# Kernel optimization log

Hardware: AMD Instinct MI355X
Metric: run time of the kernel (lower is better)

The kernel has to match this reference:

```python
import jax, jax.numpy as jnp
import numpy as np

N_EXPERT_CAPACITY = 2  # init kwarg; k = S * capacity // E


def setup_inputs() -> dict:
    key = jax.random.key(0)
    k1, k2, k3, k4 = jax.random.split(key, 4)
    B, S, D, E, F = 8, 1024, 1024, 8, 2048
    # kaiming-uniform-ish scales
    x = jax.random.normal(k1, (B, S, D), dtype=jnp.float32)
    choice_w = jax.random.uniform(k2, (E, D), dtype=jnp.float32, minval=-1.0, maxval=1.0) * (1.0 / np.sqrt(D))
    w1 = jax.random.uniform(k3, (E, D, F), dtype=jnp.float32, minval=-1.0, maxval=1.0) * (1.0 / np.sqrt(D))
    w2 = jax.random.uniform(k4, (E, F, D), dtype=jnp.float32, minval=-1.0, maxval=1.0) * (1.0 / np.sqrt(F))
    return {"x": x, "choice_w": choice_w, "w1": w1, "w2": w2}


def reference(x, choice_w, w1, w2):
    B, S, D = x.shape
    E = choice_w.shape[0]
    k = S * N_EXPERT_CAPACITY // E  # tokens per expert (expert-choice)
    # router softmax over experts: [B, S, E]
    probs = jax.nn.softmax(jnp.einsum('bsd,ed->bse', x, choice_w), axis=-1)
    # each expert picks its top-k tokens: G, I are [B, E, k]
    G, I = jax.lax.top_k(jnp.swapaxes(probs, -1, -2), k)
    # dispatch: gather tokens instead of one-hot matmul (same math)
    x_in = jnp.take_along_axis(x[:, None, :, :], I[..., None], axis=2)  # [B, E, k, D]
    # per-expert MLP with SiLU
    h = jax.nn.silu(jnp.einsum('bekd,edf->bekf', x_in, w1))  # [B, E, k, F]
    x_mlp = jnp.einsum('bekf,efd->bekd', h, w2)              # [B, E, k, D]
    # combine: weighted scatter-add back to token positions (equals P,G,x_mlp einsum)
    b_idx = jnp.arange(B)[:, None, None]  # [B,1,1] broadcasts with I [B,E,k]
    out = jnp.zeros_like(x).at[b_idx, I].add(G[..., None] * x_mlp)
    return out
```

## Files before the change

### kernel.cpp

```cpp
#include <hip/hip_runtime.h>
#include <hip/hip_bf16.h>
#include <math.h>

#define B_   8
#define S_   1024
#define D_   1024
#define E_   8
#define F_   2048
#define KCAP 256

typedef __bf16 bf16x8 __attribute__((ext_vector_type(8)));
typedef float  floatx4 __attribute__((ext_vector_type(4)));
typedef unsigned short ushortx8 __attribute__((ext_vector_type(8)));

__device__ __forceinline__ unsigned short f2b(float f) {
    union { float f; unsigned int u; } v; v.f = f;
    unsigned int u = v.u;
    u += 0x7fffu + ((u >> 16) & 1u);
    return (unsigned short)(u >> 16);
}
__device__ __forceinline__ float b2f(unsigned short u) {
    union { unsigned int u; float f; } v; v.u = ((unsigned)u) << 16; return v.f;
}

__device__ __forceinline__ void gl_lds16(const void* g, void* l) {
    __builtin_amdgcn_global_load_lds(
        (const __attribute__((address_space(1))) void*)g,
        (__attribute__((address_space(3))) void*)l, 16, 0, 0);
}

__device__ __forceinline__ unsigned long long topk_key(float p, int s) {
    return (((unsigned long long)__float_as_uint(p)) << 10) | (unsigned)(S_ - 1 - s);
}

__global__ void router_kernel(const float* __restrict__ x, const float* __restrict__ cw,
                              float* __restrict__ probs, unsigned short* __restrict__ xb) {
    int gid  = blockIdx.x * 256 + threadIdx.x;
    int wave = gid >> 6;
    int lane = gid & 63;
    int b = wave >> 10;
    int s = wave & (S_ - 1);
    const float* xrow = x + ((size_t)b * S_ + s) * D_;
    unsigned short* xbrow = xb + ((size_t)b * S_ + s) * D_;
    float acc[E_];
#pragma unroll
    for (int e = 0; e < E_; e++) acc[e] = 0.f;
#pragma unroll
    for (int it = 0; it < D_ / 256; it++) {
        int i = it * 256 + lane * 4;
        float4 xv = *(const float4*)(xrow + i);
        ushort4 o;
        o.x = f2b(xv.x); o.y = f2b(xv.y); o.z = f2b(xv.z); o.w = f2b(xv.w);
        *(ushort4*)(xbrow + i) = o;
#pragma unroll
        for (int e = 0; e < E_; e++) {
            float4 wv = *(const float4*)(cw + e * D_ + i);
            acc[e] = fmaf(xv.x, wv.x, fmaf(xv.y, wv.y, fmaf(xv.z, wv.z, fmaf(xv.w, wv.w, acc[e]))));
        }
    }
#pragma unroll
    for (int e = 0; e < E_; e++) {
        float v = acc[e];
#pragma unroll
        for (int off = 32; off >= 1; off >>= 1) v += __shfl_down(v, off, 64);
        acc[e] = v;
    }
    if (lane == 0) {
        float m = acc[0];
#pragma unroll
        for (int e = 1; e < E_; e++) m = fmaxf(m, acc[e]);
        float sum = 0.f;
#pragma unroll
        for (int e = 0; e < E_; e++) { acc[e] = __expf(acc[e] - m); sum += acc[e]; }
        float inv = 1.f / sum;
#pragma unroll
        for (int e = 0; e < E_; e++) probs[((size_t)b * E_ + e) * S_ + s] = acc[e] * inv;
    }
}

union PrepSm {
    float tile[2][128][33];
    unsigned long long keys[S_];
};

#define PREP_DECODE(T, INP, OUTP, RV, CV, C0, R0) do { \
    int t_ = (T); \
    if (t_ < 4096) { \
        int e_ = t_ >> 9, tt_ = t_ & 511; \
        INP = w1 + (size_t)e_ * D_ * F_;  OUTP = w1t + (size_t)e_ * D_ * F_; \
        RV = D_; CV = F_; C0 = (tt_ & 63) * 32; R0 = (tt_ >> 6) * 128; \
    } else { \
        int t2_ = t_ - 4096; \
        int e_ = t2_ >> 9, tt_ = t2_ & 511; \
        INP = w2 + (size_t)e_ * D_ * F_;  OUTP = w2t + (size_t)e_ * D_ * F_; \
        RV = F_; CV = D_; C0 = (tt_ & 31) * 32; R0 = (tt_ >> 5) * 128; \
    } \
} while (0)

__global__ void prep_kernel(const float* __restrict__ w1, const float* __restrict__ w2,
                            unsigned short* __restrict__ w1t, unsigned short* __restrict__ w2t,
                            const float* __restrict__ probs, int* __restrict__ I,
                            float* __restrict__ G, unsigned short* __restrict__ Pmap) {
    const int bid = blockIdx.x;
    const int tid = threadIdx.x;
    __shared__ PrepSm sm;

    if (bid < B_ * E_) {
        const int be = bid;
        const int b = be >> 3, e = be & 7;
        const float* rowp = probs + (size_t)be * S_;
#pragma unroll
        for (int q = 0; q < 4; q++) {
            const int s = q * 256 + tid;
            sm.keys[s] = topk_key(rowp[s], s);
            Pmap[((size_t)(b * S_ + s)) * E_ + e] = 0;
        }
        __syncthreads();
        unsigned long long my[4];
        int r[4] = {0, 0, 0, 0};
#pragma unroll
        for (int q = 0; q < 4; q++) my[q] = sm.keys[q * 256 + tid];
#pragma unroll 8
        for (int t = 0; t < S_; t++) {
            const unsigned long long kt = sm.keys[t];
#pragma unroll
            for (int q = 0; q < 4; q++) r[q] += (kt > my[q]);
        }
#pragma unroll
        for (int q = 0; q < 4; q++) {
            if (r[q] < KCAP) {
                const int s = q * 256 + tid;
                I[be * KCAP + r[q]] = s;
                G[be * KCAP + r[q]] = rowp[s];
                Pmap[((size_t)(b * S_ + s)) * E_ + e] = (unsigned short)(r[q] + 1);
            }
        }
        return;
    }

    const int tb   = bid - B_ * E_;
    const int lrow = tid >> 3;
    const int seg  = tid & 7;
    const int c    = tid >> 3;
    const int k    = tid & 7;

    const float* inp; unsigned short* outp; int R, C, c0, r0;
    PREP_DECODE(tb, inp, outp, R, C, c0, r0);
    float4 v[4];
#pragma unroll
    for (int i = 0; i < 4; i++)
        v[i] = *(const float4*)(inp + (size_t)(r0 + lrow + i * 32) * C + c0 + seg * 4);

    int buf = 0;
    for (int T = tb; T < 8192; T += 768) {
        unsigned short* oute = outp;
        const int Rr = R, cc0 = c0, rr0 = r0;

#pragma unroll
        for (int i = 0; i < 4; i++) {
            const int rr = lrow + i * 32;
            sm.tile[buf][rr][seg * 4 + 0] = v[i].x;
            sm.tile[buf][rr][seg * 4 + 1] = v[i].y;
            sm.tile[buf][rr][seg * 4 + 2] = v[i].z;
            sm.tile[buf][rr][seg * 4 + 3] = v[i].w;
        }
        if (T + 768 < 8192) {
            PREP_DECODE(T + 768, inp, outp, R, C, c0, r0);
#pragma unroll
            for (int i = 0; i < 4; i++)
                v[i] = *(const float4*)(inp + (size_t)(r0 + lrow + i * 32) * C + c0 + seg * 4);
        }
        __builtin_amdgcn_sched_barrier(0);
        asm volatile("s_waitcnt lgkmcnt(0)" ::: "memory");
        __builtin_amdgcn_s_barrier();
        __builtin_amdgcn_sched_barrier(0);
#pragma unroll
        for (int srep = 0; srep < 2; srep++) {
            const int s8 = k + srep * 8;
            ushortx8 o;
#pragma unroll
            for (int j = 0; j < 8; j++) o[j] = f2b(sm.tile[buf][s8 * 8 + j][c]);
            *(ushortx8*)(oute + (size_t)(cc0 + c) * Rr + rr0 + s8 * 8) = o;
        }
        buf ^= 1;
    }
}


__global__ __launch_bounds__(256, 4) void gemm1_kernel(
    const unsigned short* __restrict__ xb,
    const unsigned short* __restrict__ w1t,
    const int* __restrict__ I,
    unsigned short* __restrict__ H)
{
    const int g  = blockIdx.x;
    const int e  = g & 7;
    const int rr = g >> 3;
    const int b  = rr >> 5;
    const int t5 = rr & 31;
    const int be = b * 8 + e;
    const int mt = t5 & 1;
    const int nt = t5 >> 1;
    const int tid = threadIdx.x;

    __shared__ __align__(16) unsigned short Asm[128 * 64];
    __shared__ __align__(16) unsigned short Bsm[128 * 64];
    __shared__ unsigned int ArowS[128];

    if (tid < 128) {
        int tok = I[(size_t)be * KCAP + mt * 128 + tid];
        ArowS[tid] = (unsigned)((b * S_ + tok) * D_);
    }
    __syncthreads();

    const int r8   = tid >> 3;
    const int kseg = (tid & 7) ^ (r8 & 7);
    unsigned aoffW[4];
#pragma unroll
    for (int w = 0; w < 4; w++) aoffW[w] = ArowS[w * 32 + r8] + kseg * 8;
    const size_t boff0 = ((size_t)e * F_ + nt * 128 + r8) * D_ + kseg * 8;

    const int lane = tid & 63;
    const int wv   = tid >> 6;
    const int wm   = (wv & 1) * 64;
    const int wn   = (wv >> 1) * 64;
    const int l15  = lane & 15;
    const int quad = lane >> 4;
    const int x0   = (quad ^ (l15 & 7)) * 8;

    int aoffs[4], boffs[4];
#pragma unroll
    for (int i = 0; i < 4; i++) {
        aoffs[i] = (wm + i * 16 + l15) * 64 + x0;
        boffs[i] = (wn + i * 16 + l15) * 64 + x0;
    }

    floatx4 acc[4][4];
#pragma unroll
    for (int i = 0; i < 4; i++)
#pragma unroll
        for (int j = 0; j < 4; j++) acc[i][j] = (floatx4){0.f, 0.f, 0.f, 0.f};

    for (int k0 = 0; k0 < D_; k0 += 64) {
#pragma unroll
        for (int w = 0; w < 4; w++) {
            gl_lds16(xb  + aoffW[w] + k0,                    &Asm[(w * 256 + tid) * 8]);
            gl_lds16(w1t + boff0 + (size_t)w * 32 * D_ + k0, &Bsm[(w * 256 + tid) * 8]);
        }
        __syncthreads();
        bf16x8 af[4], bfr[4];
#pragma unroll
        for (int i = 0; i < 4; i++) {
            af[i]  = *(const bf16x8*)&Asm[aoffs[i]];
            bfr[i] = *(const bf16x8*)&Bsm[boffs[i]];
        }
#pragma unroll
        for (int i = 0; i < 4; i++)
#pragma unroll
            for (int j = 0; j < 4; j++)
                acc[i][j] = __builtin_amdgcn_mfma_f32_16x16x32_bf16(af[i], bfr[j], acc[i][j], 0, 0, 0);
#pragma unroll
        for (int i = 0; i < 4; i++) {
            af[i]  = *(const bf16x8*)&Asm[aoffs[i] ^ 32];
            bfr[i] = *(const bf16x8*)&Bsm[boffs[i] ^ 32];
        }
#pragma unroll
        for (int i = 0; i < 4; i++)
#pragma unroll
            for (int j = 0; j < 4; j++)
                acc[i][j] = __builtin_amdgcn_mfma_f32_16x16x32_bf16(af[i], bfr[j], acc[i][j], 0, 0, 0);
        __syncthreads();
    }

    unsigned short* Hbe = H + (size_t)be * KCAP * F_;
#pragma unroll
    for (int i = 0; i < 4; i++) {
#pragma unroll
        for (int r = 0; r < 4; r++) {
            int m = mt * 128 + wm + i * 16 + quad * 4 + r;
            unsigned short* hrow = Hbe + (size_t)m * F_ + nt * 128;
#pragma unroll
            for (int j = 0; j < 4; j++) {
                float v = acc[i][j][r];
                float sv = v / (1.f + __expf(-v));
                hrow[wn + j * 16 + l15] = f2b(sv);
            }
        }
    }
}

__global__ __launch_bounds__(256, 4) void gemm2_kernel(
    const unsigned short* __restrict__ H,
    const unsigned short* __restrict__ w2t,
    unsigned short* __restrict__ xmlp)
{
    const int g  = blockIdx.x;
    const int e  = g & 7;
    const int rr = g >> 3;
    const int b  = rr >> 4;
    const int t4 = rr & 15;
    const int be = b * 8 + e;
    const int mt = t4 & 1;
    const int nt = t4 >> 1;
    const int tid = threadIdx.x;

    __shared__ __align__(16) unsigned short Asm2[128 * 64];
    __shared__ __align__(16) unsigned short Bsm2[128 * 64];

    const int r8   = tid >> 3;
    const int kseg = (tid & 7) ^ (r8 & 7);
    const size_t aoff0 = ((size_t)be * KCAP + mt * 128 + r8) * F_ + kseg * 8;
    const size_t boff0 = ((size_t)e * D_ + nt * 128 + r8) * F_ + kseg * 8;

    const int lane = tid & 63;
    const int wv   = tid >> 6;
    const int wm   = (wv & 1) * 64;
    const int wn   = (wv >> 1) * 64;
    const int l15  = lane & 15;
    const int quad = lane >> 4;
    const int x0   = (quad ^ (l15 & 7)) * 8;

    int aoffs[4], boffs[4];
#pragma unroll
    for (int i = 0; i < 4; i++) {
        aoffs[i] = (wm + i * 16 + l15) * 64 + x0;
        boffs[i] = (wn + i * 16 + l15) * 64 + x0;
    }

    floatx4 acc[4][4];
#pragma unroll
    for (int i = 0; i < 4; i++)
#pragma unroll
        for (int j = 0; j < 4; j++) acc[i][j] = (floatx4){0.f, 0.f, 0.f, 0.f};

    for (int k0 = 0; k0 < F_; k0 += 64) {
#pragma unroll
        for (int w = 0; w < 4; w++) {
            gl_lds16(H   + aoff0 + (size_t)w * 32 * F_ + k0, &Asm2[(w * 256 + tid) * 8]);
            gl_lds16(w2t + boff0 + (size_t)w * 32 * F_ + k0, &Bsm2[(w * 256 + tid) * 8]);
        }
        __syncthreads();
        bf16x8 af[4], bfr[4];
#pragma unroll
        for (int i = 0; i < 4; i++) {
            af[i]  = *(const bf16x8*)&Asm2[aoffs[i]];
            bfr[i] = *(const bf16x8*)&Bsm2[boffs[i]];
        }
#pragma unroll
        for (int i = 0; i < 4; i++)
#pragma unroll
            for (int j = 0; j < 4; j++)
                acc[i][j] = __builtin_amdgcn_mfma_f32_16x16x32_bf16(af[i], bfr[j], acc[i][j], 0, 0, 0);
#pragma unroll
        for (int i = 0; i < 4; i++) {
            af[i]  = *(const bf16x8*)&Asm2[aoffs[i] ^ 32];
            bfr[i] = *(const bf16x8*)&Bsm2[boffs[i] ^ 32];
        }
#pragma unroll
        for (int i = 0; i < 4; i++)
#pragma unroll
            for (int j = 0; j < 4; j++)
                acc[i][j] = __builtin_amdgcn_mfma_f32_16x16x32_bf16(af[i], bfr[j], acc[i][j], 0, 0, 0);
        __syncthreads();
    }

    unsigned short* Xbe = xmlp + (size_t)be * KCAP * D_;
#pragma unroll
    for (int i = 0; i < 4; i++) {
#pragma unroll
        for (int r = 0; r < 4; r++) {
            int m = mt * 128 + wm + i * 16 + quad * 4 + r;
            unsigned short* orow = Xbe + (size_t)m * D_ + nt * 128;
#pragma unroll
            for (int j = 0; j < 4; j++)
                orow[wn + j * 16 + l15] = f2b(acc[i][j][r]);
        }
    }
}

__global__ void combine_kernel(const unsigned short* __restrict__ xmlp,
                               const unsigned short* __restrict__ Pmap,
                               const float* __restrict__ G,
                               float* __restrict__ out) {
    int gid  = blockIdx.x * 256 + threadIdx.x;
    int wave = gid >> 6;
    int lane = gid & 63;
    int b = wave >> 10;
    float acc[16];
#pragma unroll
    for (int i = 0; i < 16; i++) acc[i] = 0.f;
    const unsigned short* pm = Pmap + (size_t)wave * E_;
#pragma unroll
    for (int e = 0; e < E_; e++) {
        int pe = pm[e];
        if (pe) {
            int beslot = (b * E_ + e) * KCAP + (pe - 1);
            float g = G[beslot];
            const unsigned short* rw = xmlp + (size_t)beslot * D_ + lane * 16;
            ushortx8 r0 = *(const ushortx8*)(rw);
            ushortx8 r1 = *(const ushortx8*)(rw + 8);
#pragma unroll
            for (int i = 0; i < 8; i++) {
                acc[i]     = fmaf(g, b2f(r0[i]), acc[i]);
                acc[8 + i] = fmaf(g, b2f(r1[i]), acc[8 + i]);
            }
        }
    }
    float* orow = out + (size_t)wave * D_ + lane * 16;
    ((float4*)orow)[0] = make_float4(acc[0],  acc[1],  acc[2],  acc[3]);
    ((float4*)orow)[1] = make_float4(acc[4],  acc[5],  acc[6],  acc[7]);
    ((float4*)orow)[2] = make_float4(acc[8],  acc[9],  acc[10], acc[11]);
    ((float4*)orow)[3] = make_float4(acc[12], acc[13], acc[14], acc[15]);
}

extern "C" void kernel_launch(void* const* d_in, const int* in_sizes, int n_in,
                              void* d_out, int out_size, void* d_ws, size_t ws_size,
                              hipStream_t stream) {
    const float* x  = (const float*)d_in[0];
    const float* cw = (const float*)d_in[1];
    const float* w1 = (const float*)d_in[2];
    const float* w2 = (const float*)d_in[3];
    float* out = (float*)d_out;

    char* ws = (char*)d_ws;
    float*          probs = (float*)(ws);
    int*            Ibuf  = (int*)(ws + 262144);
    float*          Gbuf  = (float*)(ws + 327680);
    unsigned short* Pmap  = (unsigned short*)(ws + 393216);
    unsigned short* xb    = (unsigned short*)(ws + 524288);
    unsigned short* w1t   = (unsigned short*)(ws + 17301504);
    unsigned short* xmlp  = w1t;
    unsigned short* w2t   = (unsigned short*)(ws + 50855936);
    unsigned short* Hbuf  = (unsigned short*)(ws + 84410368);

    router_kernel<<<(B_ * S_ * 64) / 256, 256, 0, stream>>>(x, cw, probs, xb);
    prep_kernel<<<B_ * E_ + 768, 256, 0, stream>>>(w1, w2, w1t, w2t, probs, Ibuf, Gbuf, Pmap);
    gemm1_kernel<<<B_ * E_ * 2 * (F_ / 128), 256, 0, stream>>>(xb, w1t, Ibuf, Hbuf);
    gemm2_kernel<<<B_ * E_ * 2 * (D_ / 128), 256, 0, stream>>>(Hbuf, w2t, xmlp);
    combine_kernel<<<(B_ * S_ * 64) / 256, 256, 0, stream>>>(xmlp, Pmap, Gbuf, out);
}
```

Baseline: 355.4 us.

## Overlap weight transposes with router and gemm1 by splitting prep work across kernels

The w1 transpose now runs inside the router kernel as extra persistent blocks, and the w2 transpose runs inside the gemm1 kernel as extra blocks. Top-k selection moves into its own small kernel. The goal is to hide the weight conversion and transpose traffic behind the router and gemm1 work instead of running it as a serial prep stage. In exchange, the transpose blocks compete with gemm1 for CUs and bandwidth, gemm1 now uses a larger shared-memory union, and there is one extra kernel launch.

```diff
diff --git a/kernel.cpp b/kernel.cpp
--- a/kernel.cpp
+++ b/kernel.cpp
@@ -32,56 +32,6 @@
 __device__ __forceinline__ unsigned long long topk_key(float p, int s) {
     return (((unsigned long long)__float_as_uint(p)) << 10) | (unsigned)(S_ - 1 - s);
 }
-
-__global__ void router_kernel(const float* __restrict__ x, const float* __restrict__ cw,
-                              float* __restrict__ probs, unsigned short* __restrict__ xb) {
-    int gid  = blockIdx.x * 256 + threadIdx.x;
-    int wave = gid >> 6;
-    int lane = gid & 63;
-    int b = wave >> 10;
-    int s = wave & (S_ - 1);
-    const float* xrow = x + ((size_t)b * S_ + s) * D_;
-    unsigned short* xbrow = xb + ((size_t)b * S_ + s) * D_;
-    float acc[E_];
-#pragma unroll
-    for (int e = 0; e < E_; e++) acc[e] = 0.f;
-#pragma unroll
-    for (int it = 0; it < D_ / 256; it++) {
-        int i = it * 256 + lane * 4;
-        float4 xv = *(const float4*)(xrow + i);
-        ushort4 o;
-        o.x = f2b(xv.x); o.y = f2b(xv.y); o.z = f2b(xv.z); o.w = f2b(xv.w);
-        *(ushort4*)(xbrow + i) = o;
-#pragma unroll
-        for (int e = 0; e < E_; e++) {
-            float4 wv = *(const float4*)(cw + e * D_ + i);
-            acc[e] = fmaf(xv.x, wv.x, fmaf(xv.y, wv.y, fmaf(xv.z, wv.z, fmaf(xv.w, wv.w, acc[e]))));
-        }
-    }
-#pragma unroll
-    for (int e = 0; e < E_; e++) {
-        float v = acc[e];
-#pragma unroll
-        for (int off = 32; off >= 1; off >>= 1) v += __shfl_down(v, off, 64);
-        acc[e] = v;
-    }
-    if (lane == 0) {
-        float m = acc[0];
-#pragma unroll
-        for (int e = 1; e < E_; e++) m = fmaxf(m, acc[e]);
-        float sum = 0.f;
-#pragma unroll
-        for (int e = 0; e < E_; e++) { acc[e] = __expf(acc[e] - m); sum += acc[e]; }
-        float inv = 1.f / sum;
-#pragma unroll
-        for (int e = 0; e < E_; e++) probs[((size_t)b * E_ + e) * S_ + s] = acc[e] * inv;
-    }
-}
-
-union PrepSm {
-    float tile[2][128][33];
-    unsigned long long keys[S_];
-};
 
 #define PREP_DECODE(T, INP, OUTP, RV, CV, C0, R0) do { \
     int t_ = (T); \
@@ -97,75 +47,37 @@
     } \
 } while (0)
 
-__global__ void prep_kernel(const float* __restrict__ w1, const float* __restrict__ w2,
-                            unsigned short* __restrict__ w1t, unsigned short* __restrict__ w2t,
-                            const float* __restrict__ probs, int* __restrict__ I,
-                            float* __restrict__ G, unsigned short* __restrict__ Pmap) {
-    const int bid = blockIdx.x;
-    const int tid = threadIdx.x;
-    __shared__ PrepSm sm;
-
-    if (bid < B_ * E_) {
-        const int be = bid;
-        const int b = be >> 3, e = be & 7;
-        const float* rowp = probs + (size_t)be * S_;
-#pragma unroll
-        for (int q = 0; q < 4; q++) {
-            const int s = q * 256 + tid;
-            sm.keys[s] = topk_key(rowp[s], s);
-            Pmap[((size_t)(b * S_ + s)) * E_ + e] = 0;
-        }
-        __syncthreads();
-        unsigned long long my[4];
-        int r[4] = {0, 0, 0, 0};
-#pragma unroll
-        for (int q = 0; q < 4; q++) my[q] = sm.keys[q * 256 + tid];
-#pragma unroll 8
-        for (int t = 0; t < S_; t++) {
-            const unsigned long long kt = sm.keys[t];
-#pragma unroll
-            for (int q = 0; q < 4; q++) r[q] += (kt > my[q]);
-        }
-#pragma unroll
-        for (int q = 0; q < 4; q++) {
-            if (r[q] < KCAP) {
-                const int s = q * 256 + tid;
-                I[be * KCAP + r[q]] = s;
-                G[be * KCAP + r[q]] = rowp[s];
-                Pmap[((size_t)(b * S_ + s)) * E_ + e] = (unsigned short)(r[q] + 1);
-            }
-        }
-        return;
-    }
-
-    const int tb   = bid - B_ * E_;
+__device__ __forceinline__ void transpose_persist(
+    const float* __restrict__ w1, const float* __restrict__ w2,
+    unsigned short* __restrict__ w1t, unsigned short* __restrict__ w2t,
+    float (*tile)[128][33], int T0, int Tend, int stride, int tid)
+{
     const int lrow = tid >> 3;
     const int seg  = tid & 7;
     const int c    = tid >> 3;
     const int k    = tid & 7;
 
     const float* inp; unsigned short* outp; int R, C, c0, r0;
-    PREP_DECODE(tb, inp, outp, R, C, c0, r0);
+    PREP_DECODE(T0, inp, outp, R, C, c0, r0);
     float4 v[4];
 #pragma unroll
     for (int i = 0; i < 4; i++)
         v[i] = *(const float4*)(inp + (size_t)(r0 + lrow + i * 32) * C + c0 + seg * 4);
 
     int buf = 0;
-    for (int T = tb; T < 8192; T += 768) {
+    for (int T = T0; T < Tend; T += stride) {
         unsigned short* oute = outp;
         const int Rr = R, cc0 = c0, rr0 = r0;
-
 #pragma unroll
         for (int i = 0; i < 4; i++) {
             const int rr = lrow + i * 32;
-            sm.tile[buf][rr][seg * 4 + 0] = v[i].x;
-            sm.tile[buf][rr][seg * 4 + 1] = v[i].y;
-            sm.tile[buf][rr][seg * 4 + 2] = v[i].z;
-            sm.tile[buf][rr][seg * 4 + 3] = v[i].w;
-        }
-        if (T + 768 < 8192) {
-            PREP_DECODE(T + 768, inp, outp, R, C, c0, r0);
+            tile[buf][rr][seg * 4 + 0] = v[i].x;
+            tile[buf][rr][seg * 4 + 1] = v[i].y;
+            tile[buf][rr][seg * 4 + 2] = v[i].z;
+            tile[buf][rr][seg * 4 + 3] = v[i].w;
+        }
+        if (T + stride < Tend) {
+            PREP_DECODE(T + stride, inp, outp, R, C, c0, r0);
 #pragma unroll
             for (int i = 0; i < 4; i++)
                 v[i] = *(const float4*)(inp + (size_t)(r0 + lrow + i * 32) * C + c0 + seg * 4);
@@ -179,21 +91,131 @@
             const int s8 = k + srep * 8;
             ushortx8 o;
 #pragma unroll
-            for (int j = 0; j < 8; j++) o[j] = f2b(sm.tile[buf][s8 * 8 + j][c]);
+            for (int j = 0; j < 8; j++) o[j] = f2b(tile[buf][s8 * 8 + j][c]);
             *(ushortx8*)(oute + (size_t)(cc0 + c) * Rr + rr0 + s8 * 8) = o;
         }
         buf ^= 1;
     }
 }
 
-
-__global__ __launch_bounds__(256, 4) void gemm1_kernel(
+__global__ void router_w1t_kernel(const float* __restrict__ x, const float* __restrict__ cw,
+                                  float* __restrict__ probs, unsigned short* __restrict__ xb,
+                                  const float* __restrict__ w1, const float* __restrict__ w2,
+                                  unsigned short* __restrict__ w1t, unsigned short* __restrict__ w2t) {
+    const int bid = blockIdx.x;
+    const int tid = threadIdx.x;
+    __shared__ float tile[2][128][33];
+
+    if (bid < 384) {
+        transpose_persist(w1, w2, w1t, w2t, tile, bid, 4096, 384, tid);
+        return;
+    }
+
+    int gid  = (bid - 384) * 256 + tid;
+    int wave = gid >> 6;
+    int lane = gid & 63;
+    int b = wave >> 10;
+    int s = wave & (S_ - 1);
+    const float* xrow = x + ((size_t)b * S_ + s) * D_;
+    unsigned short* xbrow = xb + ((size_t)b * S_ + s) * D_;
+    float acc[E_];
+#pragma unroll
+    for (int e = 0; e < E_; e++) acc[e] = 0.f;
+#pragma unroll
+    for (int it = 0; it < D_ / 256; it++) {
+        int i = it * 256 + lane * 4;
+        float4 xv = *(const float4*)(xrow + i);
+        ushort4 o;
+        o.x = f2b(xv.x); o.y = f2b(xv.y); o.z = f2b(xv.z); o.w = f2b(xv.w);
+        *(ushort4*)(xbrow + i) = o;
+#pragma unroll
+        for (int e = 0; e < E_; e++) {
+            float4 wv = *(const float4*)(cw + e * D_ + i);
+            acc[e] = fmaf(xv.x, wv.x, fmaf(xv.y, wv.y, fmaf(xv.z, wv.z, fmaf(xv.w, wv.w, acc[e]))));
+        }
+    }
+#pragma unroll
+    for (int e = 0; e < E_; e++) {
+        float v = acc[e];
+#pragma unroll
+        for (int off = 32; off >= 1; off >>= 1) v += __shfl_down(v, off, 64);
+        acc[e] = v;
+    }
+    if (lane == 0) {
+        float m = acc[0];
+#pragma unroll
+        for (int e = 1; e < E_; e++) m = fmaxf(m, acc[e]);
+        float sum = 0.f;
+#pragma unroll
+        for (int e = 0; e < E_; e++) { acc[e] = __expf(acc[e] - m); sum += acc[e]; }
+        float inv = 1.f / sum;
+#pragma unroll
+        for (int e = 0; e < E_; e++) probs[((size_t)b * E_ + e) * S_ + s] = acc[e] * inv;
+    }
+}
+
+__global__ void topk_kernel(const float* __restrict__ probs, int* __restrict__ I,
+                            float* __restrict__ G, unsigned short* __restrict__ Pmap) {
+    const int be = blockIdx.x;
+    const int b = be >> 3, e = be & 7;
+    const int tid = threadIdx.x;
+    __shared__ unsigned long long keys[S_];
+    const float* rowp = probs + (size_t)be * S_;
+#pragma unroll
+    for (int q = 0; q < 4; q++) {
+        const int s = q * 256 + tid;
+        keys[s] = topk_key(rowp[s], s);
+        Pmap[((size_t)(b * S_ + s)) * E_ + e] = 0;
+    }
+    __syncthreads();
+    unsigned long long my[4];
+    int r[4] = {0, 0, 0, 0};
+#pragma unroll
+    for (int q = 0; q < 4; q++) my[q] = keys[q * 256 + tid];
+#pragma unroll 8
+    for (int t = 0; t < S_; t++) {
+        const unsigned long long kt = keys[t];
+#pragma unroll
+        for (int q = 0; q < 4; q++) r[q] += (kt > my[q]);
+    }
+#pragma unroll
+    for (int q = 0; q < 4; q++) {
+        if (r[q] < KCAP) {
+            const int s = q * 256 + tid;
+            I[be * KCAP + r[q]] = s;
+            G[be * KCAP + r[q]] = rowp[s];
+            Pmap[((size_t)(b * S_ + s)) * E_ + e] = (unsigned short)(r[q] + 1);
+        }
+    }
+}
+
+
+union GemmTransSm {
+    struct {
+        unsigned short Asm[128 * 64];
+        unsigned short Bsm[128 * 64];
+        unsigned int   ArowS[128];
+    } g;
+    float tile[2][128][33];
+};
+
+__global__ __launch_bounds__(256, 4) void gemm1_w2t_kernel(
     const unsigned short* __restrict__ xb,
-    const unsigned short* __restrict__ w1t,
+    const unsigned short* __restrict__ w1t_,
     const int* __restrict__ I,
-    unsigned short* __restrict__ H)
+    unsigned short* __restrict__ H,
+    const float* __restrict__ w1, const float* __restrict__ w2,
+    unsigned short* __restrict__ w1t, unsigned short* __restrict__ w2t)
 {
-    const int g  = blockIdx.x;
+    __shared__ __align__(16) GemmTransSm sm;
+    const int g   = blockIdx.x;
+    const int tid = threadIdx.x;
+
+    if (g >= 2048) {
+        transpose_persist(w1, w2, w1t, w2t, sm.tile, 4096 + (g - 2048), 8192, 384, tid);
+        return;
+    }
+
     const int e  = g & 7;
     const int rr = g >> 3;
     const int b  = rr >> 5;
@@ -201,15 +223,10 @@
     const int be = b * 8 + e;
     const int mt = t5 & 1;
     const int nt = t5 >> 1;
-    const int tid = threadIdx.x;
-
-    __shared__ __align__(16) unsigned short Asm[128 * 64];
-    __shared__ __align__(16) unsigned short Bsm[128 * 64];
-    __shared__ unsigned int ArowS[128];
 
     if (tid < 128) {
         int tok = I[(size_t)be * KCAP + mt * 128 + tid];
-        ArowS[tid] = (unsigned)((b * S_ + tok) * D_);
+        sm.g.ArowS[tid] = (unsigned)((b * S_ + tok) * D_);
     }
     __syncthreads();
 
@@ -217,7 +234,7 @@
     const int kseg = (tid & 7) ^ (r8 & 7);
     unsigned aoffW[4];
 #pragma unroll
-    for (int w = 0; w < 4; w++) aoffW[w] = ArowS[w * 32 + r8] + kseg * 8;
+    for (int w = 0; w < 4; w++) aoffW[w] = sm.g.ArowS[w * 32 + r8] + kseg * 8;
     const size_t boff0 = ((size_t)e * F_ + nt * 128 + r8) * D_ + kseg * 8;
 
     const int lane = tid & 63;
@@ -244,15 +261,15 @@
     for (int k0 = 0; k0 < D_; k0 += 64) {
 #pragma unroll
         for (int w = 0; w < 4; w++) {
-            gl_lds16(xb  + aoffW[w] + k0,                    &Asm[(w * 256 + tid) * 8]);
-            gl_lds16(w1t + boff0 + (size_t)w * 32 * D_ + k0, &Bsm[(w * 256 + tid) * 8]);
+            gl_lds16(xb   + aoffW[w] + k0,                    &sm.g.Asm[(w * 256 + tid) * 8]);
+            gl_lds16(w1t_ + boff0 + (size_t)w * 32 * D_ + k0, &sm.g.Bsm[(w * 256 + tid) * 8]);
         }
         __syncthreads();
         bf16x8 af[4], bfr[4];
 #pragma unroll
         for (int i = 0; i < 4; i++) {
-            af[i]  = *(const bf16x8*)&Asm[aoffs[i]];
-            bfr[i] = *(const bf16x8*)&Bsm[boffs[i]];
+            af[i]  = *(const bf16x8*)&sm.g.Asm[aoffs[i]];
+            bfr[i] = *(const bf16x8*)&sm.g.Bsm[boffs[i]];
         }
 #pragma unroll
         for (int i = 0; i < 4; i++)
@@ -261,8 +278,8 @@
                 acc[i][j] = __builtin_amdgcn_mfma_f32_16x16x32_bf16(af[i], bfr[j], acc[i][j], 0, 0, 0);
 #pragma unroll
         for (int i = 0; i < 4; i++) {
-            af[i]  = *(const bf16x8*)&Asm[aoffs[i] ^ 32];
-            bfr[i] = *(const bf16x8*)&Bsm[boffs[i] ^ 32];
+            af[i]  = *(const bf16x8*)&sm.g.Asm[aoffs[i] ^ 32];
+            bfr[i] = *(const bf16x8*)&sm.g.Bsm[boffs[i] ^ 32];
         }
 #pragma unroll
         for (int i = 0; i < 4; i++)
@@ -433,9 +450,11 @@
     unsigned short* w2t   = (unsigned short*)(ws + 50855936);
     unsigned short* Hbuf  = (unsigned short*)(ws + 84410368);
 
-    router_kernel<<<(B_ * S_ * 64) / 256, 256, 0, stream>>>(x, cw, probs, xb);
-    prep_kernel<<<B_ * E_ + 768, 256, 0, stream>>>(w1, w2, w1t, w2t, probs, Ibuf, Gbuf, Pmap);
-    gemm1_kernel<<<B_ * E_ * 2 * (F_ / 128), 256, 0, stream>>>(xb, w1t, Ibuf, Hbuf);
+    router_w1t_kernel<<<384 + (B_ * S_ * 64) / 256, 256, 0, stream>>>(
+        x, cw, probs, xb, w1, w2, w1t, w2t);
+    topk_kernel<<<B_ * E_, 256, 0, stream>>>(probs, Ibuf, Gbuf, Pmap);
+    gemm1_w2t_kernel<<<2048 + 384, 256, 0, stream>>>(
+        xb, w1t, Ibuf, Hbuf, w1, w2, w1t, w2t);
     gemm2_kernel<<<B_ * E_ * 2 * (D_ / 128), 256, 0, stream>>>(Hbuf, w2t, xmlp);
     combine_kernel<<<(B_ * S_ * 64) / 256, 256, 0, stream>>>(xmlp, Pmap, Gbuf, out);
 }
```

Result: slower. 374.0 us (+5.3%).
